# Kernel optimization log

Hardware: AMD Instinct MI355X
Metric: run time of the kernel (lower is better)

The kernel has to match this reference:

```python
import jax, jax.numpy as jnp
import numpy as np

GAMMA = 0.1
BIG = 1e10  # finite stand-in for +inf (avoids nan grads through masked lanes)


def _softmin3(a, b, c, gamma):
    # soft-min_gamma(a,b,c) = -gamma * logsumexp(-[a,b,c]/gamma)
    z = jnp.stack([a, b, c], axis=-1)
    return -gamma * jax.nn.logsumexp(-z / gamma, axis=-1)


def _soft_dtw(x, y, gamma):
    # x: [B,N,K], y: [B,M,K]; squared Euclidean pairwise distances via GEMM
    x2 = jnp.sum(x * x, axis=-1)  # [B,N]
    y2 = jnp.sum(y * y, axis=-1)  # [B,M]
    D = x2[:, :, None] + y2[:, None, :] - 2.0 * jnp.einsum('bik,bjk->bij', x, y)  # [B,N,M]
    B, n, m = D.shape
    i_idx = jnp.arange(n)

    # Anti-diagonal wavefront DP. Diagonal d holds cells (i, j=d-i).
    # Carry two previous diagonals as length-n vectors indexed by i.
    r_prev2 = jnp.full((B, n), BIG, D.dtype)                      # diag d-2
    r_prev = jnp.full((B, n), BIG, D.dtype).at[:, 0].set(D[:, 0, 0])  # diag d-1 (d=0: R[0,0]=D[0,0])

    def step(carry, d):
        r2, r1 = carry
        j = d - i_idx                      # column index per lane i
        valid = (j >= 0) & (j < m)
        jc = jnp.clip(j, 0, m - 1)
        d_vals = jnp.take_along_axis(D, jc[None, :, None], axis=2)[..., 0]  # [B,n] = D[:, i, d-i]
        pad = jnp.full((B, 1), BIG, D.dtype)
        r11 = jnp.concatenate([pad, r2[:, :-1]], axis=1)  # R[i-1, j-1]
        r10 = jnp.concatenate([pad, r1[:, :-1]], axis=1)  # R[i-1, j]
        r01 = r1                                          # R[i,   j-1]
        r_new = jnp.where(valid[None, :], d_vals + _softmin3(r11, r10, r01, gamma), BIG)
        return (r1, r_new), None

    (_, r_last), _ = jax.lax.scan(step, (r_prev2, r_prev), jnp.arange(1, n + m - 1))
    return r_last[:, n - 1]  # R[N-1, M-1] per batch element -> [B]


def setup_inputs() -> dict:
    key = jax.random.key(0)
    kx, ky = jax.random.split(key)
    B, N, M, K = 32, 1024, 1024, 64
    x = jax.random.normal(kx, (B, N, K), dtype=jnp.float32)
    y = jax.random.normal(ky, (B, M, K), dtype=jnp.float32)
    return {"x": x, "y": y}


def reference(x, y):
    # ExpressionDWTLoss.forward: soft_dtw(stack(x, -1), y); x is pre-stacked here.
    return _soft_dtw(x, y, GAMMA)
```

## Files before the change

kernel.cpp:

```cpp
#include <hip/hip_runtime.h>
#include <hip/hip_bf16.h>

#define BATCH 32
#define NN 1024
#define MM 1024
#define KK 64
#define DD 2052
#define SCALE 14.4269504088896f
#define INV_SCALE 0.0693147180559945f
#define BIGU 1.44269504e11f

typedef _Float16 h4 __attribute__((ext_vector_type(4)));
typedef float f4 __attribute__((ext_vector_type(4)));

#define LDS_BARRIER() asm volatile("s_waitcnt lgkmcnt(0)\ns_barrier" ::: "memory")

template <int DIAG>
__global__ __launch_bounds__(256) void dist_kernel(
    const float* __restrict__ x, const float* __restrict__ y,
    _Float16* __restrict__ D) {
  const int b  = blockIdx.z;
  const int ti = blockIdx.y;
  const int tj = blockIdx.x;
  const int t  = threadIdx.x;

  __shared__ float xs[64][68];
  __shared__ float ys[64][68];

  {
    const int lr = t >> 4;
    const int lc = (t & 15) * 4;
    const float* xp = x + (size_t)(b * NN + ti * 64) * KK;
    const float* yp = y + (size_t)(b * MM + tj * 64) * KK;
#pragma unroll
    for (int r = 0; r < 4; ++r) {
      const int row = lr + r * 16;
      f4 xv = *(const f4*)(xp + (size_t)row * KK + lc);
      f4 yv = *(const f4*)(yp + (size_t)row * KK + lc);
      xs[row][lc + 0] = xv[0]; xs[row][lc + 1] = xv[1];
      xs[row][lc + 2] = xv[2]; xs[row][lc + 3] = xv[3];
      ys[row][lc + 0] = yv[0]; ys[row][lc + 1] = yv[1];
      ys[row][lc + 2] = yv[2]; ys[row][lc + 3] = yv[3];
    }
  }
  __syncthreads();

  const int tx = (t & 15) * 4;
  const int ty = (t >> 4) * 4;

  float acc[4][4];
  float x2[4], y2[4];
#pragma unroll
  for (int a = 0; a < 4; ++a) {
    x2[a] = 0.f; y2[a] = 0.f;
#pragma unroll
    for (int c = 0; c < 4; ++c) acc[a][c] = 0.f;
  }

#pragma unroll 4
  for (int k = 0; k < KK; k += 4) {
    f4 xa[4], yb[4];
#pragma unroll
    for (int a = 0; a < 4; ++a) xa[a] = *(const f4*)&xs[ty + a][k];
#pragma unroll
    for (int c = 0; c < 4; ++c) yb[c] = *(const f4*)&ys[tx + c][k];
#pragma unroll
    for (int a = 0; a < 4; ++a) {
      x2[a] += xa[a][0] * xa[a][0] + xa[a][1] * xa[a][1] +
               xa[a][2] * xa[a][2] + xa[a][3] * xa[a][3];
      y2[a] += yb[a][0] * yb[a][0] + yb[a][1] * yb[a][1] +
               yb[a][2] * yb[a][2] + yb[a][3] * yb[a][3];
    }
#pragma unroll
    for (int a = 0; a < 4; ++a)
#pragma unroll
      for (int c = 0; c < 4; ++c)
        acc[a][c] += xa[a][0] * yb[c][0] + xa[a][1] * yb[c][1] +
                     xa[a][2] * yb[c][2] + xa[a][3] * yb[c][3];
  }

  if constexpr (DIAG) {
    __shared__ _Float16 dbuf[127][66];
#pragma unroll
    for (int a = 0; a < 4; ++a)
#pragma unroll
      for (int c = 0; c < 4; ++c) {
        const int li = ty + a, lj = tx + c;
        dbuf[li + lj][li] =
            (_Float16)((x2[a] + y2[c] - 2.0f * acc[a][c]) * SCALE);
      }
    __syncthreads();

    _Float16* Db = D + (size_t)b * DD * NN;
    const int wave = t >> 6, lane = t & 63;
    const int d0 = ti * 64 + tj * 64;
    const int c0 = ti * 64;
    for (int ld = wave; ld < 127; ld += 4) {
      const int lo = ld > 63 ? ld - 63 : 0;
      const int hi = ld < 63 ? ld : 63;
      const int li = lo + lane;
      if (li <= hi)
        Db[(size_t)(d0 + ld) * NN + c0 + li] = dbuf[ld][li];
    }
  } else {
    _Float16* Dp = D + (size_t)b * NN * MM + (size_t)(ti * 64 + ty) * MM +
                   (tj * 64 + tx);
#pragma unroll
    for (int a = 0; a < 4; ++a) {
      h4 v;
#pragma unroll
      for (int c = 0; c < 4; ++c)
        v[c] = (_Float16)((x2[a] + y2[c] - 2.0f * acc[a][c]) * SCALE);
      *(h4*)(Dp + (size_t)a * MM) = v;
    }
  }
}

__global__ __launch_bounds__(256) void dtw_diag_kernel(
    const _Float16* __restrict__ Dd, float* __restrict__ out) {
  const int b  = blockIdx.x;
  const int t  = threadIdx.x;
  const int i0 = t * 4;
  const _Float16* Db = Dd + (size_t)b * DD * NN;

  __shared__ float lex[2][8][256];

  float w1[8], w2[8];
#pragma unroll
  for (int j = 0; j < 8; ++j) { w1[j] = BIGU; w2[j] = BIGU; }
  if (t == 0) w1[4] = (float)Db[0];

  h4 Al0, Al1, Al2, Ah0, Ah1, Ah2, Ah3;
  h4 Bl0, Bl1, Bl2, Bh0, Bh1, Bh2, Bh3;

#define STAGE(L0, L1, L2, H0, H1, H2, H3, D0S)                                \
  do {                                                                        \
    const long long _o = (long long)(D0S)*NN;                                 \
    L0 = *(const h4*)(Db + (size_t)(_o + i0 - 4));                            \
    L1 = *(const h4*)(Db + (size_t)(_o + NN + i0 - 4));                       \
    L2 = *(const h4*)(Db + (size_t)(_o + 2 * NN + i0 - 4));                   \
    H0 = *(const h4*)(Db + (size_t)(_o + i0));                                \
    H1 = *(const h4*)(Db + (size_t)(_o + NN + i0));                           \
    H2 = *(const h4*)(Db + (size_t)(_o + 2 * NN + i0));                       \
    H3 = *(const h4*)(Db + (size_t)(_o + 3 * NN + i0));                       \
  } while (0)

#define EXCHANGE(PAR)                                                         \
  do {                                                                        \
    lex[PAR][0][t] = w1[4]; lex[PAR][1][t] = w1[5];                           \
    lex[PAR][2][t] = w1[6]; lex[PAR][3][t] = w1[7];                           \
    lex[PAR][4][t] = w2[4]; lex[PAR][5][t] = w2[5];                           \
    lex[PAR][6][t] = w2[6]; lex[PAR][7][t] = w2[7];                           \
    LDS_BARRIER();                                                            \
    if (t > 0) {                                                              \
      w1[0] = lex[PAR][0][t - 1]; w1[1] = lex[PAR][1][t - 1];                 \
      w1[2] = lex[PAR][2][t - 1]; w1[3] = lex[PAR][3][t - 1];                 \
      w2[0] = lex[PAR][4][t - 1]; w2[1] = lex[PAR][5][t - 1];                 \
      w2[2] = lex[PAR][6][t - 1]; w2[3] = lex[PAR][7][t - 1];                 \
    }                                                                         \
  } while (0)

#define CELL(J, DV, DG)                                                       \
  do {                                                                        \
    const int _ri = i0 - 4 + (J);                                             \
    const bool _v =                                                           \
        ((unsigned)_ri < (unsigned)NN) && ((unsigned)((DG)-_ri) < (unsigned)MM); \
    const float _a = w2[(J)-1], _b = w1[(J)-1], _c = w1[(J)];                 \
    const float _mn = fminf(fminf(_a, _b), _c);                               \
    const float _md = __builtin_amdgcn_fmed3f(_a, _b, _c);                    \
    const float _mx = fmaxf(fmaxf(_a, _b), _c);                               \
    const float _s = 1.0f + __builtin_amdgcn_exp2f(_mn - _md) +               \
                     __builtin_amdgcn_exp2f(_mn - _mx);                       \
    w2[(J)] = w1[(J)];                                                        \
    w1[(J)] = _v ? (float)(DV) + _mn - __builtin_amdgcn_logf(_s) : BIGU;      \
  } while (0)

#define BLOCK4(PAR, L0, L1, L2, H0, H1, H2, H3, D0V)                          \
  do {                                                                        \
    EXCHANGE(PAR);                                                            \
    const int _d = (D0V);                                                     \
                                                  \
    CELL(7, H0[3], _d); CELL(6, H0[2], _d); CELL(5, H0[1], _d);               \
    CELL(4, H0[0], _d); CELL(3, L0[3], _d); CELL(2, L0[2], _d);               \
    CELL(1, L0[1], _d);                                                       \
                                                  \
    CELL(7, H1[3], _d + 1); CELL(6, H1[2], _d + 1); CELL(5, H1[1], _d + 1);   \
    CELL(4, H1[0], _d + 1); CELL(3, L1[3], _d + 1); CELL(2, L1[2], _d + 1);   \
                                                  \
    CELL(7, H2[3], _d + 2); CELL(6, H2[2], _d + 2); CELL(5, H2[1], _d + 2);   \
    CELL(4, H2[0], _d + 2); CELL(3, L2[3], _d + 2);                           \
                                                  \
    CELL(7, H3[3], _d + 3); CELL(6, H3[2], _d + 3); CELL(5, H3[1], _d + 3);   \
    CELL(4, H3[0], _d + 3);                                                   \
  } while (0)

  STAGE(Al0, Al1, Al2, Ah0, Ah1, Ah2, Ah3, 1);
  STAGE(Bl0, Bl1, Bl2, Bh0, Bh1, Bh2, Bh3, 5);

  int d0 = 1;
  for (int n = 0; n < 255; ++n) {
    BLOCK4(0, Al0, Al1, Al2, Ah0, Ah1, Ah2, Ah3, d0);
    STAGE(Al0, Al1, Al2, Ah0, Ah1, Ah2, Ah3, d0 + 8);
    BLOCK4(1, Bl0, Bl1, Bl2, Bh0, Bh1, Bh2, Bh3, d0 + 4);
    STAGE(Bl0, Bl1, Bl2, Bh0, Bh1, Bh2, Bh3, d0 + 12);
    d0 += 8;
  }
  BLOCK4(0, Al0, Al1, Al2, Ah0, Ah1, Ah2, Ah3, 2041);

  EXCHANGE(1);
  CELL(7, Bh0[3], 2045); CELL(6, Bh0[2], 2045); CELL(5, Bh0[1], 2045);
  CELL(4, Bh0[0], 2045); CELL(3, Bl0[3], 2045); CELL(2, Bl0[2], 2045);
  CELL(1, Bl0[1], 2045);
  CELL(7, Bh1[3], 2046); CELL(6, Bh1[2], 2046); CELL(5, Bh1[1], 2046);
  CELL(4, Bh1[0], 2046); CELL(3, Bl1[3], 2046); CELL(2, Bl1[2], 2046);

  if (t == 255) out[b] = w1[7] * INV_SCALE;

#undef STAGE
#undef EXCHANGE
#undef CELL
#undef BLOCK4
}

__global__ __launch_bounds__(256) void dtw_row_kernel(
    const _Float16* __restrict__ D, float* __restrict__ out) {
  const int b  = blockIdx.x;
  const int t  = threadIdx.x;
  const int i0 = t * 4;
  const _Float16* Dr = D + (size_t)(b * NN + i0) * MM;

  __shared__ float lx[2][256];

  float r1[4], r2[4];
#pragma unroll
  for (int k = 0; k < 4; ++k) { r1[k] = BIGU; r2[k] = BIGU; }
  if (t == 0) r1[0] = (float)Dr[0];

  float dv[4], dvn[4];
#pragma unroll
  for (int k = 0; k < 4; ++k) {
    int j1 = 1 - (i0 + k);
    int jc1 = j1 < 0 ? 0 : (j1 > MM - 1 ? MM - 1 : j1);
    dv[k] = (float)Dr[(size_t)k * MM + jc1];
    int j2 = 2 - (i0 + k);
    int jc2 = j2 < 0 ? 0 : (j2 > MM - 1 ? MM - 1 : j2);
    dvn[k] = (float)Dr[(size_t)k * MM + jc2];
  }

  float nl1_prev = BIGU;

  for (int d = 1; d <= NN + MM - 2; ++d) {
    const int pp = d & 1;
    lx[pp][t] = r1[3];
    __syncthreads();
    const float nl1 = (t > 0) ? lx[pp][t - 1] : BIGU;
    const float nl2 = nl1_prev;

    float rn[4];
#pragma unroll
    for (int k = 0; k < 4; ++k) {
      const int j = d - (i0 + k);
      const float a  = k ? r2[k - 1] : nl2;
      const float bb = k ? r1[k - 1] : nl1;
      const float c  = r1[k];
      const float m  = fminf(fminf(a, bb), c);
      const float s  = exp2f(m - a) + exp2f(m - bb) + exp2f(m - c);
      const float sm = m - log2f(s);
      rn[k] = (j >= 0 && j < MM) ? dv[k] + sm : BIGU;
    }

    nl1_prev = nl1;
#pragma unroll
    for (int k = 0; k < 4; ++k) { r2[k] = r1[k]; r1[k] = rn[k]; dv[k] = dvn[k]; }

    const int dn = d + 2;
#pragma unroll
    for (int k = 0; k < 4; ++k) {
      int j = dn - (i0 + k);
      int jc = j < 0 ? 0 : (j > MM - 1 ? MM - 1 : j);
      dvn[k] = (float)Dr[(size_t)k * MM + jc];
    }
  }

  if (t == 255) out[b] = r1[3] * INV_SCALE;
}

extern "C" void kernel_launch(void* const* d_in, const int* in_sizes, int n_in,
                              void* d_out, int out_size, void* d_ws,
                              size_t ws_size, hipStream_t stream) {
  const float* x = (const float*)d_in[0];
  const float* y = (const float*)d_in[1];
  float* out = (float*)d_out;

  const size_t need_diag = (size_t)BATCH * DD * NN * sizeof(_Float16);
  const size_t need_row  = (size_t)BATCH * NN * MM * sizeof(_Float16);
  dim3 g1(MM / 64, NN / 64, BATCH);

  if (ws_size >= need_diag) {
    _Float16* Dd = (_Float16*)d_ws;
    dist_kernel<1><<<g1, 256, 0, stream>>>(x, y, Dd);
    dtw_diag_kernel<<<BATCH, 256, 0, stream>>>(Dd, out);
  } else if (ws_size >= need_row) {
    _Float16* D = (_Float16*)d_ws;
    dist_kernel<0><<<g1, 256, 0, stream>>>(x, y, D);
    dtw_row_kernel<<<BATCH, 256, 0, stream>>>(D, out);
  }
}
```

Measured before the change: 930.7 us.

## Widen DTW diagonal halo to two neighbours, halving barrier count

The diagonal-wavefront DTW kernel now exchanges halo values with both the neighbour one thread away and the neighbour two threads away, holding 12 cells per thread instead of 8. This lets each exchange cover 8 anti-diagonals instead of 4, so there are half as many LDS barriers. The cost is more redundant softmin work in the triangular halo region, more global loads per stage (24 h4 vectors instead of 7), and higher register pressure from the larger staged buffers.

```diff
diff --git a/kernel.cpp b/kernel.cpp
--- a/kernel.cpp
+++ b/kernel.cpp
@@ -125,44 +125,54 @@
 
   __shared__ float lex[2][8][256];
 
-  float w1[8], w2[8];
-#pragma unroll
-  for (int j = 0; j < 8; ++j) { w1[j] = BIGU; w2[j] = BIGU; }
-  if (t == 0) w1[4] = (float)Db[0];
-
-  h4 Al0, Al1, Al2, Ah0, Ah1, Ah2, Ah3;
-  h4 Bl0, Bl1, Bl2, Bh0, Bh1, Bh2, Bh3;
-
-#define STAGE(L0, L1, L2, H0, H1, H2, H3, D0S)                                \
-  do {                                                                        \
-    const long long _o = (long long)(D0S)*NN;                                 \
-    L0 = *(const h4*)(Db + (size_t)(_o + i0 - 4));                            \
-    L1 = *(const h4*)(Db + (size_t)(_o + NN + i0 - 4));                       \
-    L2 = *(const h4*)(Db + (size_t)(_o + 2 * NN + i0 - 4));                   \
-    H0 = *(const h4*)(Db + (size_t)(_o + i0));                                \
-    H1 = *(const h4*)(Db + (size_t)(_o + NN + i0));                           \
-    H2 = *(const h4*)(Db + (size_t)(_o + 2 * NN + i0));                       \
-    H3 = *(const h4*)(Db + (size_t)(_o + 3 * NN + i0));                       \
+  float w1[12], w2[12];
+#pragma unroll
+  for (int j = 0; j < 12; ++j) { w1[j] = BIGU; w2[j] = BIGU; }
+  if (t == 0) w1[8] = (float)Db[0];
+
+  h4 GA[3][8], GB[3][8];
+
+#define STAGE(G, D0S)                                                         \
+  do {                                                                        \
+    const long long _o = (long long)(D0S) * NN;                               \
+    _Pragma("unroll")                                                         \
+    for (int _q = 0; _q < 8; ++_q) {                                          \
+      G[0][_q] = *(const h4*)(Db + (size_t)(_o + _q * NN + i0 - 8));          \
+      G[1][_q] = *(const h4*)(Db + (size_t)(_o + _q * NN + i0 - 4));          \
+      G[2][_q] = *(const h4*)(Db + (size_t)(_o + _q * NN + i0));              \
+    }                                                                         \
   } while (0)
 
 #define EXCHANGE(PAR)                                                         \
   do {                                                                        \
-    lex[PAR][0][t] = w1[4]; lex[PAR][1][t] = w1[5];                           \
-    lex[PAR][2][t] = w1[6]; lex[PAR][3][t] = w1[7];                           \
-    lex[PAR][4][t] = w2[4]; lex[PAR][5][t] = w2[5];                           \
-    lex[PAR][6][t] = w2[6]; lex[PAR][7][t] = w2[7];                           \
+    lex[PAR][0][t] = w1[8];  lex[PAR][1][t] = w1[9];                          \
+    lex[PAR][2][t] = w1[10]; lex[PAR][3][t] = w1[11];                         \
+    lex[PAR][4][t] = w2[8];  lex[PAR][5][t] = w2[9];                          \
+    lex[PAR][6][t] = w2[10]; lex[PAR][7][t] = w2[11];                         \
     LDS_BARRIER();                                                            \
-    if (t > 0) {                                                              \
-      w1[0] = lex[PAR][0][t - 1]; w1[1] = lex[PAR][1][t - 1];                 \
-      w1[2] = lex[PAR][2][t - 1]; w1[3] = lex[PAR][3][t - 1];                 \
-      w2[0] = lex[PAR][4][t - 1]; w2[1] = lex[PAR][5][t - 1];                 \
-      w2[2] = lex[PAR][6][t - 1]; w2[3] = lex[PAR][7][t - 1];                 \
+    if (t >= 2) {                                                             \
+      w1[0] = lex[PAR][0][t - 2]; w1[1] = lex[PAR][1][t - 2];                 \
+      w1[2] = lex[PAR][2][t - 2]; w1[3] = lex[PAR][3][t - 2];                 \
+      w2[0] = lex[PAR][4][t - 2]; w2[1] = lex[PAR][5][t - 2];                 \
+      w2[2] = lex[PAR][6][t - 2]; w2[3] = lex[PAR][7][t - 2];                 \
+    } else {                                                                  \
+      w1[0] = w1[1] = w1[2] = w1[3] = BIGU;                                   \
+      w2[0] = w2[1] = w2[2] = w2[3] = BIGU;                                   \
     }                                                                         \
+    if (t >= 1) {                                                             \
+      w1[4] = lex[PAR][0][t - 1]; w1[5] = lex[PAR][1][t - 1];                 \
+      w1[6] = lex[PAR][2][t - 1]; w1[7] = lex[PAR][3][t - 1];                 \
+      w2[4] = lex[PAR][4][t - 1]; w2[5] = lex[PAR][5][t - 1];                 \
+      w2[6] = lex[PAR][6][t - 1]; w2[7] = lex[PAR][7][t - 1];                 \
+    } else {                                                                  \
+      w1[4] = w1[5] = w1[6] = w1[7] = BIGU;                                   \
+      w2[4] = w2[5] = w2[6] = w2[7] = BIGU;                                   \
+    }                                                                         \
   } while (0)
 
 #define CELL(J, DV, DG)                                                       \
   do {                                                                        \
-    const int _ri = i0 - 4 + (J);                                             \
+    const int _ri = i0 - 8 + (J);                                             \
     const bool _v =                                                           \
         ((unsigned)_ri < (unsigned)NN) && ((unsigned)((DG)-_ri) < (unsigned)MM); \
     const float _a = w2[(J)-1], _b = w1[(J)-1], _c = w1[(J)];                 \
@@ -175,51 +185,65 @@
     w1[(J)] = _v ? (float)(DV) + _mn - __builtin_amdgcn_logf(_s) : BIGU;      \
   } while (0)
 
-#define BLOCK4(PAR, L0, L1, L2, H0, H1, H2, H3, D0V)                          \
+#define CG(G, Q, J, DG) CELL(J, G[(J) >> 2][Q][(J)&3], DG)
+
+#define STEP(G, Q, JMIN, DG)                                                  \
+  do {                                                                        \
+    if (11 >= (JMIN)) CG(G, Q, 11, DG);                                       \
+    if (10 >= (JMIN)) CG(G, Q, 10, DG);                                       \
+    if (9 >= (JMIN))  CG(G, Q, 9, DG);                                        \
+    if (8 >= (JMIN))  CG(G, Q, 8, DG);                                        \
+    if (7 >= (JMIN))  CG(G, Q, 7, DG);                                        \
+    if (6 >= (JMIN))  CG(G, Q, 6, DG);                                        \
+    if (5 >= (JMIN))  CG(G, Q, 5, DG);                                        \
+    if (4 >= (JMIN))  CG(G, Q, 4, DG);                                        \
+    if (3 >= (JMIN))  CG(G, Q, 3, DG);                                        \
+    if (2 >= (JMIN))  CG(G, Q, 2, DG);                                        \
+    if (1 >= (JMIN))  CG(G, Q, 1, DG);                                        \
+  } while (0)
+
+#define BLOCK8(PAR, G, D0V)                                                   \
   do {                                                                        \
     EXCHANGE(PAR);                                                            \
-    const int _d = (D0V);                                                     \
-                                                  \
-    CELL(7, H0[3], _d); CELL(6, H0[2], _d); CELL(5, H0[1], _d);               \
-    CELL(4, H0[0], _d); CELL(3, L0[3], _d); CELL(2, L0[2], _d);               \
-    CELL(1, L0[1], _d);                                                       \
-                                                  \
-    CELL(7, H1[3], _d + 1); CELL(6, H1[2], _d + 1); CELL(5, H1[1], _d + 1);   \
-    CELL(4, H1[0], _d + 1); CELL(3, L1[3], _d + 1); CELL(2, L1[2], _d + 1);   \
-                                                  \
-    CELL(7, H2[3], _d + 2); CELL(6, H2[2], _d + 2); CELL(5, H2[1], _d + 2);   \
-    CELL(4, H2[0], _d + 2); CELL(3, L2[3], _d + 2);                           \
-                                                  \
-    CELL(7, H3[3], _d + 3); CELL(6, H3[2], _d + 3); CELL(5, H3[1], _d + 3);   \
-    CELL(4, H3[0], _d + 3);                                                   \
-  } while (0)
-
-  STAGE(Al0, Al1, Al2, Ah0, Ah1, Ah2, Ah3, 1);
-  STAGE(Bl0, Bl1, Bl2, Bh0, Bh1, Bh2, Bh3, 5);
+    STEP(G, 0, 1, (D0V));                                                     \
+    STEP(G, 1, 2, (D0V) + 1);                                                 \
+    STEP(G, 2, 3, (D0V) + 2);                                                 \
+    STEP(G, 3, 4, (D0V) + 3);                                                 \
+    STEP(G, 4, 5, (D0V) + 4);                                                 \
+    STEP(G, 5, 6, (D0V) + 5);                                                 \
+    STEP(G, 6, 7, (D0V) + 6);                                                 \
+    STEP(G, 7, 8, (D0V) + 7);                                                 \
+  } while (0)
+
+  STAGE(GA, 1);
+  STAGE(GB, 9);
 
   int d0 = 1;
-  for (int n = 0; n < 255; ++n) {
-    BLOCK4(0, Al0, Al1, Al2, Ah0, Ah1, Ah2, Ah3, d0);
-    STAGE(Al0, Al1, Al2, Ah0, Ah1, Ah2, Ah3, d0 + 8);
-    BLOCK4(1, Bl0, Bl1, Bl2, Bh0, Bh1, Bh2, Bh3, d0 + 4);
-    STAGE(Bl0, Bl1, Bl2, Bh0, Bh1, Bh2, Bh3, d0 + 12);
-    d0 += 8;
-  }
-  BLOCK4(0, Al0, Al1, Al2, Ah0, Ah1, Ah2, Ah3, 2041);
+  for (int n = 0; n < 127; ++n) {
+    BLOCK8(0, GA, d0);
+    STAGE(GA, d0 + 16);
+    BLOCK8(1, GB, d0 + 8);
+    STAGE(GB, d0 + 24);
+    d0 += 16;
+  }
+  BLOCK8(0, GA, 2033);
 
   EXCHANGE(1);
-  CELL(7, Bh0[3], 2045); CELL(6, Bh0[2], 2045); CELL(5, Bh0[1], 2045);
-  CELL(4, Bh0[0], 2045); CELL(3, Bl0[3], 2045); CELL(2, Bl0[2], 2045);
-  CELL(1, Bl0[1], 2045);
-  CELL(7, Bh1[3], 2046); CELL(6, Bh1[2], 2046); CELL(5, Bh1[1], 2046);
-  CELL(4, Bh1[0], 2046); CELL(3, Bl1[3], 2046); CELL(2, Bl1[2], 2046);
-
-  if (t == 255) out[b] = w1[7] * INV_SCALE;
+  STEP(GB, 0, 1, 2041);
+  STEP(GB, 1, 2, 2042);
+  STEP(GB, 2, 3, 2043);
+  STEP(GB, 3, 4, 2044);
+  STEP(GB, 4, 5, 2045);
+  STEP(GB, 5, 6, 2046);
+
+  if (t == 255) out[b] = w1[11] * INV_SCALE;
 
 #undef STAGE
 #undef EXCHANGE
 #undef CELL
-#undef BLOCK4
+#undef CG
+#undef STEP
+#undef BLOCK8
 }
 
 __global__ __launch_bounds__(256) void dtw_row_kernel(
```

After: 1.018 ms. 9.4% more time.
